# Kernel tuning notes

Hardware: AMD Instinct MI355X
Metric: run time of the kernel (lower is better)

Reference implementation:

```python
import math
import jax, jax.numpy as jnp
import numpy as np

C, H, W, N = 128, 64, 64, 32


def setup_inputs() -> dict:
    key = jax.random.key(0)
    k = jax.random.split(key, 6)
    std = 0.02
    return {
        "x": jax.random.normal(k[0], (N, C, H, W), dtype=jnp.float32),
        # p_3: 1x1 conv, weight [out=C, in=3C]
        "w3": jax.random.normal(k[1], (C, 3 * C), dtype=jnp.float32) * std,
        "p5_w": jax.random.normal(k[2], (1, 1, H, W), dtype=jnp.float32) * std,
        # p_6: conv (3,1), dilation (3,1), weight [O=C, I=C, 3, 1]
        "w6": jax.random.normal(k[3], (C, C, 3, 1), dtype=jnp.float32) * std,
        "p8_w": jax.random.normal(k[4], (1, C, 1, 1), dtype=jnp.float32) * std,
        "p12_w": jax.random.normal(k[5], (1, 1, 3, H, 1), dtype=jnp.float32) * std,
    }


def reference(x, w3, p5_w, w6, p8_w, p12_w):
    n, c, h, w = x.shape
    # F.unfold(x, (1,3), dilation=(1,2), padding=(0,2)) -> taps at w-2, w, w+2 (zero padded)
    xp = jnp.pad(x, ((0, 0), (0, 0), (0, 0), (2, 2)))
    t1 = jnp.stack([xp[..., 0:w], xp[..., 2:w + 2], xp[..., 4:w + 4]], axis=2)  # [n,c,3,h,w]
    t2 = t1.max(axis=2)                                                          # [n,c,h,w]
    # p_3: 1x1 conv over 3c channels
    t3 = jnp.einsum('nkhw,ok->nohw', t1.reshape(n, c * 3, h, w), w3)            # [n,c,h,w]
    t4 = jnp.maximum(t3[:, :, None], t1)                                         # [n,c,3,h,w]
    t5 = p5_w * t2
    # p_6: (3,1) conv, dilation (3,1), padding (3,0) -> same spatial size
    t6 = jax.lax.conv_general_dilated(
        t5, w6, window_strides=(1, 1), padding=((3, 3), (0, 0)),
        rhs_dilation=(3, 1), dimension_numbers=('NCHW', 'OIHW', 'NCHW'))         # [n,c,h,w]
    t7 = jnp.maximum(x, t6)
    t8 = p8_w * t7
    # bmm: [n,c,hw] x [n,hw,3c] -> [n,c,3c]
    t9 = jnp.einsum('ncp,nkp->nck', t8.reshape(n, c, h * w),
                    t1.reshape(n, c * 3, h * w)) / math.sqrt(h * w)
    t10 = t7[:, :, None] + t4                                                    # [n,c,3,h,w]
    t11 = jnp.maximum(t6[:, :, None], t10)                                       # [n,c,3,h,w]
    t12 = p12_w * t11
    # bmm: [n,hw,3c] x [n,3c,c] -> [n,hw,c]
    t13 = jnp.einsum('nkp,nck->npc', t12.reshape(n, c * 3, h * w), t9) / math.sqrt(c * 3)
    return t13.reshape(n, h, w, c).transpose(0, 3, 1, 2)                         # [n,c,h,w]
```

## Files before the change

### kernel.cpp

```cpp
#include <hip/hip_runtime.h>

#define C_   128
#define P_   4096
#define K3   384
#define CP   (C_*P_)
#define NB_  32

typedef __attribute__((ext_vector_type(8))) short short8;
typedef __attribute__((ext_vector_type(4))) short short4v;
typedef __attribute__((ext_vector_type(4))) float f32x4;

__device__ __forceinline__ short f2bf(float f) {
  union { float f; unsigned u; } v; v.f = f;
  unsigned r = v.u + 0x7fffu + ((v.u >> 16) & 1u);
  return (short)(r >> 16);
}
__device__ __forceinline__ float bf2f(short b) {
  union { unsigned u; float f; } v; v.u = ((unsigned)(unsigned short)b) << 16;
  return v.f;
}
__device__ __forceinline__ void gl_lds16(const void* g, void* l) {
  __builtin_amdgcn_global_load_lds(
      (const __attribute__((address_space(1))) unsigned int*)g,
      (__attribute__((address_space(3))) unsigned int*)l, 16, 0, 0);
}

__global__ __launch_bounds__(256) void prep_kernel(const float* __restrict__ w3,
                                                   const float* __restrict__ w6,
                                                   short* __restrict__ w3p,
                                                   short* __restrict__ w6p) {
  int idx = blockIdx.x * 256 + threadIdx.x;
  int m = idx / K3, kp = idx - m * K3;
  int j = kp >> 7, c = kp & 127;
  w3p[idx] = f2bf(w3[m * K3 + c * 3 + j]);
  w6p[idx] = f2bf(w6[m * K3 + c * 3 + j]);
}

__global__ __launch_bounds__(256) void xk_kernel(const float* __restrict__ x,
                                                 short* __restrict__ xb,
                                                 short* __restrict__ xT) {
  int b = blockIdx.x;
  int pt = b & 63, ct = (b >> 6) & 1, n = b >> 7;
  int p0 = pt * 64, c0 = ct * 64;
  const float* xn = x + (size_t)n * CP;
  short* xbn = xb + (size_t)n * CP;
  short* xTn = xT + (size_t)n * CP;
  __shared__ short Ls[64][68];
  int tid = threadIdx.x;
#pragma unroll
  for (int it = 0; it < 4; ++it) {
    int fid = tid + it * 256;
    int i = fid >> 4, j4 = fid & 15;
    f32x4 v = *(const f32x4*)(xn + (c0 + i) * P_ + p0 + j4 * 4);
    short4v s;
#pragma unroll
    for (int r = 0; r < 4; ++r) s[r] = f2bf(v[r]);
    *(short4v*)(xbn + (c0 + i) * P_ + p0 + j4 * 4) = s;
    *(short4v*)(&Ls[i][j4 * 4]) = s;
  }
  __syncthreads();
#pragma unroll
  for (int it = 0; it < 4; ++it) {
    int oid = tid + it * 256;
    int pr = oid >> 4, cg = oid & 15, cb = cg * 4;
    short4v a;
#pragma unroll
    for (int r = 0; r < 4; ++r) a[r] = Ls[cb + r][pr];
    *(short4v*)(xTn + (p0 + pr) * C_ + c0 + cb) = a;
  }
}

__global__ __launch_bounds__(256) void g12_kernel(const short* __restrict__ w3p,
                                                  const short* __restrict__ w6p,
                                                  const float* __restrict__ p5,
                                                  const short* __restrict__ xT,
                                                  short* __restrict__ t3T,
                                                  short* __restrict__ t6T,
                                                  short* __restrict__ t7T) {
  int blk = blockIdx.x;
  int role = blk & 1;
  int b = blk >> 1;
  int n = b >> 5, pt = b & 31, p0 = pt * 128;
  int tid = threadIdx.x, lane = tid & 63, wv = tid >> 6;
  int wm = (wv & 1) * 64, wp = (wv >> 1) * 64;
  const short* Ap = role ? w3p : w6p;
  const short* xTn = xT + (size_t)n * CP;
  __shared__ __align__(16) short As[4][128][8];
  __shared__ __align__(16) short Bs[4][128][8];
  f32x4 acc[4][4] = {};
  for (int ks = 0; ks < 12; ++ks) {
    int k0 = ks * 32;
    int jr = ks >> 2;
    __syncthreads();
#pragma unroll
    for (int it = 0; it < 2; ++it) {
      int slot = tid + it * 256;
      int q = slot >> 7, m = slot & 127;
      gl_lds16(Ap + m * K3 + k0 + q * 8, &As[q][m][0]);
    }
#pragma unroll
    for (int it = 0; it < 2; ++it) {
      int slot = tid + it * 256;
      int q = slot & 3, pc = slot >> 2;
      int p = p0 + pc;
      int c0k = ((ks & 3) * 32) + q * 8;
      short8 zero = {};
      short8 v;
      if (role) {
        int d = 2 * (jr - 1);
        int wd = (p & 63) + d;
        bool valid = (wd >= 0 && wd < 64);
        int prc = min(max(p + d, 0), P_ - 1);
        v = *(const short8*)(xTn + (size_t)prc * C_ + c0k);
        if (!valid) v = zero;
      } else {
        int pr = p + 192 * (jr - 1);
        bool rv = (pr >= 0 && pr < P_);
        int prc = min(max(pr, 0), P_ - 1);
        int w2 = prc & 63;
        const short* rb = xTn + (size_t)prc * C_ + c0k;
        short8 vm = *(const short8*)rb;
        short8 vl = (w2 >= 2) ? *(const short8*)(rb - 2 * C_) : zero;
        short8 vr = (w2 < 62) ? *(const short8*)(rb + 2 * C_) : zero;
        float p5v = p5[prc];
#pragma unroll
        for (int jj = 0; jj < 8; ++jj)
          v[jj] = f2bf(p5v * fmaxf(fmaxf(bf2f(vl[jj]), bf2f(vm[jj])), bf2f(vr[jj])));
        if (!rv) v = zero;
      }
      *(short8*)(&Bs[q][pc][0]) = v;
    }
    __syncthreads();
    int row = lane & 15, q = lane >> 4;
    short8 a[4], bb[4];
#pragma unroll
    for (int im = 0; im < 4; ++im) a[im] = *(const short8*)(&As[q][wm + im * 16 + row][0]);
#pragma unroll
    for (int ip = 0; ip < 4; ++ip) bb[ip] = *(const short8*)(&Bs[q][wp + ip * 16 + row][0]);
#pragma unroll
    for (int im = 0; im < 4; ++im)
#pragma unroll
      for (int ip = 0; ip < 4; ++ip)
        acc[im][ip] = __builtin_amdgcn_mfma_f32_16x16x32_bf16(a[im], bb[ip], acc[im][ip], 0, 0, 0);
  }
  int col = lane & 15, rq = lane >> 4;
  if (role) {
    short* t3Tn = t3T + (size_t)n * CP;
#pragma unroll
    for (int im = 0; im < 4; ++im)
#pragma unroll
      for (int ip = 0; ip < 4; ++ip) {
        int m0 = wm + im * 16 + rq * 4;
        int p = p0 + wp + ip * 16 + col;
        short4v s;
#pragma unroll
        for (int r = 0; r < 4; ++r) s[r] = f2bf(acc[im][ip][r]);
        *(short4v*)(t3Tn + (size_t)p * C_ + m0) = s;
      }
  } else {
    short* t6Tn = t6T + (size_t)n * CP;
    short* t7Tn = t7T + (size_t)n * CP;
#pragma unroll
    for (int im = 0; im < 4; ++im)
#pragma unroll
      for (int ip = 0; ip < 4; ++ip) {
        int m0 = wm + im * 16 + rq * 4;
        int p = p0 + wp + ip * 16 + col;
        short4v ax = *(const short4v*)(xTn + (size_t)p * C_ + m0);
        short4v s6, s7;
#pragma unroll
        for (int r = 0; r < 4; ++r) {
          float t6v = acc[im][ip][r];
          float t7v = fmaxf(bf2f(ax[r]), t6v);
          s6[r] = f2bf(t6v);
          s7[r] = f2bf(t7v);
        }
        *(short4v*)(t6Tn + (size_t)p * C_ + m0) = s6;
        *(short4v*)(t7Tn + (size_t)p * C_ + m0) = s7;
      }
  }
}

__global__ __launch_bounds__(256) void g3_kernel(const short* __restrict__ xb,
                                                 const short* __restrict__ t7T,
                                                 float* __restrict__ t9) {
  int blk = blockIdx.x;
  int nb = blk % 3;
  int tmp = blk / 3;
  int n = tmp & 31, sk = tmp >> 5;
  int d = 2 * (nb - 1);
  int tid = threadIdx.x, lane = tid & 63, wv = tid >> 6;
  int wm = (wv & 1) * 64, wp = (wv >> 1) * 64;
  const short* xbn = xb + (size_t)n * CP;
  const short* t7n = t7T + (size_t)n * CP;
  __shared__ __align__(16) short As[4][128][8];
  __shared__ __align__(16) short Bs[4][128][8];
  f32x4 acc[4][4] = {};
  for (int ks = 0; ks < 16; ++ks) {
    int pp0 = sk * 512 + ks * 32;
    __syncthreads();
#pragma unroll
    for (int it = 0; it < 2; ++it) {
      int slot = tid + it * 256;
      int q = slot >> 7, kc = slot & 127;
      int pb = pp0 + q * 8;
      const int* src = (const int*)(xbn + kc * P_ + pb + d);
      union { int i[4]; short8 s; } u;
#pragma unroll
      for (int t = 0; t < 4; ++t) u.i[t] = src[t];
      short8 v = u.s;
      int w0 = pb & 63;
      if (nb == 0) { if (w0 == 0) { v[0] = 0; v[1] = 0; } }
      else if (nb == 2) { if (w0 == 56) { v[6] = 0; v[7] = 0; } }
      *(short8*)(&As[q][kc][0]) = v;
    }
#pragma unroll
    for (int it = 0; it < 2; ++it) {
      int slot = tid + it * 256;
      int q = slot >> 7, cc = slot & 127;
      const short* bp = t7n + (size_t)(pp0 + q * 8) * C_ + cc;
      short8 v;
#pragma unroll
      for (int j = 0; j < 8; ++j) v[j] = bp[j * C_];
      *(short8*)(&Bs[q][cc][0]) = v;
    }
    __syncthreads();
    int row = lane & 15, q = lane >> 4;
    short8 a[4], bb[4];
#pragma unroll
    for (int im = 0; im < 4; ++im) a[im] = *(const short8*)(&As[q][wm + im * 16 + row][0]);
#pragma unroll
    for (int ip = 0; ip < 4; ++ip) bb[ip] = *(const short8*)(&Bs[q][wp + ip * 16 + row][0]);
#pragma unroll
    for (int im = 0; im < 4; ++im)
#pragma unroll
      for (int ip = 0; ip < 4; ++ip)
        acc[im][ip] = __builtin_amdgcn_mfma_f32_16x16x32_bf16(a[im], bb[ip], acc[im][ip], 0, 0, 0);
  }
  int col = lane & 15, rq = lane >> 4;
  float* t9n = t9 + (size_t)n * (K3 * C_);
#pragma unroll
  for (int im = 0; im < 4; ++im)
#pragma unroll
    for (int ip = 0; ip < 4; ++ip)
#pragma unroll
      for (int r = 0; r < 4; ++r) {
        int kp = nb * 128 + wm + im * 16 + rq * 4 + r;
        int c = wp + ip * 16 + col;
        atomicAdd(&t9n[(size_t)kp * C_ + c], acc[im][ip][r]);
      }
}

__global__ __launch_bounds__(256) void g4_kernel(const float* __restrict__ t9,
                                                 const float* __restrict__ p8,
                                                 const float* __restrict__ p12,
                                                 const short* __restrict__ t3T,
                                                 const short* __restrict__ t6T,
                                                 const short* __restrict__ t7T,
                                                 const short* __restrict__ xT,
                                                 float* __restrict__ out) {
  int b = blockIdx.x;
  int n = b >> 5, pt = b & 31, p0 = pt * 128;
  int tid = threadIdx.x, lane = tid & 63, wv = tid >> 6;
  int wm = (wv & 1) * 64, wp = (wv >> 1) * 64;
  const float* t9n = t9 + (size_t)n * (K3 * C_);
  const short* t3n = t3T + (size_t)n * CP;
  const short* t6n = t6T + (size_t)n * CP;
  const short* t7n = t7T + (size_t)n * CP;
  const short* xTn = xT + (size_t)n * CP;
  const float INV = 1.0f / (64.0f * 19.5959179423f);
  __shared__ __align__(16) short As[4][128][8];
  __shared__ __align__(16) short Bs[4][128][8];
  f32x4 acc[4][4] = {};
  for (int ks = 0; ks < 12; ++ks) {
    int k0 = ks * 32;
    int j = ks >> 2, d = 2 * (j - 1);
    __syncthreads();
#pragma unroll
    for (int it = 0; it < 2; ++it) {
      int slot = tid + it * 256;
      int q = slot >> 7, m = slot & 127;
      float sc = p8[m] * INV;
      short8 v;
#pragma unroll
      for (int jj = 0; jj < 8; ++jj)
        v[jj] = f2bf(t9n[(size_t)(k0 + q * 8 + jj) * C_ + m] * sc);
      *(short8*)(&As[q][m][0]) = v;
    }
#pragma unroll
    for (int it = 0; it < 2; ++it) {
      int slot = tid + it * 256;
      int q = slot & 3, pc = slot >> 2;
      int p = p0 + pc;
      int c0k = ((ks & 3) * 32) + q * 8;
      float s12 = p12[j * 64 + (p >> 6)];
      size_t base = (size_t)p * C_ + c0k;
      short8 a6 = *(const short8*)(t6n + base);
      short8 a7 = *(const short8*)(t7n + base);
      short8 a3 = *(const short8*)(t3n + base);
      int wd = (p & 63) + d;
      bool valid = (wd >= 0 && wd < 64);
      int pr = min(max(p + d, 0), P_ - 1);
      short8 ax = *(const short8*)(xTn + (size_t)pr * C_ + c0k);
      short8 zero = {};
      if (!valid) ax = zero;
      short8 v;
#pragma unroll
      for (int jj = 0; jj < 8; ++jj) {
        float t11 = fmaxf(bf2f(a6[jj]), bf2f(a7[jj]) + fmaxf(bf2f(a3[jj]), bf2f(ax[jj])));
        v[jj] = f2bf(s12 * t11);
      }
      *(short8*)(&Bs[q][pc][0]) = v;
    }
    __syncthreads();
    int row = lane & 15, q = lane >> 4;
    short8 a[4], bb[4];
#pragma unroll
    for (int im = 0; im < 4; ++im) a[im] = *(const short8*)(&As[q][wm + im * 16 + row][0]);
#pragma unroll
    for (int ip = 0; ip < 4; ++ip) bb[ip] = *(const short8*)(&Bs[q][wp + ip * 16 + row][0]);
#pragma unroll
    for (int im = 0; im < 4; ++im)
#pragma unroll
      for (int ip = 0; ip < 4; ++ip)
        acc[im][ip] = __builtin_amdgcn_mfma_f32_16x16x32_bf16(a[im], bb[ip], acc[im][ip], 0, 0, 0);
  }
  int col = lane & 15, rq = lane >> 4;
#pragma unroll
  for (int im = 0; im < 4; ++im)
#pragma unroll
    for (int ip = 0; ip < 4; ++ip)
#pragma unroll
      for (int r = 0; r < 4; ++r) {
        int m = wm + im * 16 + rq * 4 + r;
        int p = p0 + wp + ip * 16 + col;
        out[(size_t)n * CP + m * P_ + p] = acc[im][ip][r];
      }
}

extern "C" void kernel_launch(void* const* d_in, const int* in_sizes, int n_in,
                              void* d_out, int out_size, void* d_ws, size_t ws_size,
                              hipStream_t stream) {
  const float* x   = (const float*)d_in[0];
  const float* w3  = (const float*)d_in[1];
  const float* p5  = (const float*)d_in[2];
  const float* w6  = (const float*)d_in[3];
  const float* p8  = (const float*)d_in[4];
  const float* p12 = (const float*)d_in[5];
  float* out = (float*)d_out;

  char* ws = (char*)d_ws;
  const size_t RB = (size_t)NB_ * CP * 2;
  size_t off = 256;
  short* xb  = (short*)(ws + off); off += RB;
  short* xT  = (short*)(ws + off); off += RB;
  short* t3T = (short*)(ws + off); off += RB;
  short* t6T = (short*)(ws + off); off += RB;
  short* t7T = (short*)(ws + off); off += RB;
  float* t9  = (float*)(ws + off); off += (size_t)NB_ * K3 * C_ * 4;
  short* w3p = (short*)(ws + off); off += 49152 * 2;
  short* w6p = (short*)(ws + off); off += 49152 * 2;

  prep_kernel<<<192, 256, 0, stream>>>(w3, w6, w3p, w6p);
  xk_kernel<<<4096, 256, 0, stream>>>(x, xb, xT);
  g12_kernel<<<2048, 256, 0, stream>>>(w3p, w6p, p5, xT, t3T, t6T, t7T);
  hipMemsetAsync(t9, 0, (size_t)NB_ * K3 * C_ * sizeof(float), stream);
  g3_kernel<<<768, 256, 0, stream>>>(xb, t7T, t9);
  g4_kernel<<<1024, 256, 0, stream>>>(t9, p8, p12, t3T, t6T, t7T, xT, out);
}
```

Baseline: 446.9 us.

## Double-buffer LDS tiles in all GEMM kernels and fold weight prep into xk kernel

Each of the three GEMM kernels now double-buffers its A and B shared-memory tiles. The next k-step's global loads go into registers or are issued as async global-to-LDS copies before the current step's MFMAs, so only one barrier per step is needed. g12's role-1 B path now uses direct global-to-LDS loads, with a zero buffer standing in for padded taps. The separate weight-prep launch is merged into xk_kernel as extra blocks, which removes one launch. In exchange, LDS use doubles to 32KB per block and register pressure rises from the prefetch registers, which may lower occupancy.

```diff
diff --git a/kernel.cpp b/kernel.cpp
--- a/kernel.cpp
+++ b/kernel.cpp
@@ -25,21 +25,40 @@
       (__attribute__((address_space(3))) unsigned int*)l, 16, 0, 0);
 }
 
-__global__ __launch_bounds__(256) void prep_kernel(const float* __restrict__ w3,
-                                                   const float* __restrict__ w6,
-                                                   short* __restrict__ w3p,
-                                                   short* __restrict__ w6p) {
-  int idx = blockIdx.x * 256 + threadIdx.x;
-  int m = idx / K3, kp = idx - m * K3;
-  int j = kp >> 7, c = kp & 127;
-  w3p[idx] = f2bf(w3[m * K3 + c * 3 + j]);
-  w6p[idx] = f2bf(w6[m * K3 + c * 3 + j]);
+__device__ __forceinline__ void mfma_phase(const short (*As_)[128][8],
+                                           const short (*Bs_)[128][8],
+                                           f32x4 acc[4][4], int lane, int wm, int wp) {
+  int row = lane & 15, q = lane >> 4;
+  short8 a[4], bb[4];
+#pragma unroll
+  for (int im = 0; im < 4; ++im) a[im] = *(const short8*)(&As_[q][wm + im * 16 + row][0]);
+#pragma unroll
+  for (int ip = 0; ip < 4; ++ip) bb[ip] = *(const short8*)(&Bs_[q][wp + ip * 16 + row][0]);
+#pragma unroll
+  for (int im = 0; im < 4; ++im)
+#pragma unroll
+    for (int ip = 0; ip < 4; ++ip)
+      acc[im][ip] = __builtin_amdgcn_mfma_f32_16x16x32_bf16(a[im], bb[ip], acc[im][ip], 0, 0, 0);
 }
 
 __global__ __launch_bounds__(256) void xk_kernel(const float* __restrict__ x,
+                                                 const float* __restrict__ w3,
+                                                 const float* __restrict__ w6,
                                                  short* __restrict__ xb,
-                                                 short* __restrict__ xT) {
+                                                 short* __restrict__ xT,
+                                                 short* __restrict__ w3p,
+                                                 short* __restrict__ w6p,
+                                                 short* __restrict__ zbuf) {
   int b = blockIdx.x;
+  if (b >= 4096) {
+    int idx = (b - 4096) * 256 + threadIdx.x;
+    int m = idx / K3, kp = idx - m * K3;
+    int j = kp >> 7, c = kp & 127;
+    w3p[idx] = f2bf(w3[m * K3 + c * 3 + j]);
+    w6p[idx] = f2bf(w6[m * K3 + c * 3 + j]);
+    if (idx < 16) zbuf[idx] = 0;
+    return;
+  }
   int pt = b & 63, ct = (b >> 6) & 1, n = b >> 7;
   int p0 = pt * 64, c0 = ct * 64;
   const float* xn = x + (size_t)n * CP;
@@ -74,6 +93,7 @@
                                                   const short* __restrict__ w6p,
                                                   const float* __restrict__ p5,
                                                   const short* __restrict__ xT,
+                                                  const short* __restrict__ zbuf,
                                                   short* __restrict__ t3T,
                                                   short* __restrict__ t6T,
                                                   short* __restrict__ t7T) {
@@ -85,64 +105,75 @@
   int wm = (wv & 1) * 64, wp = (wv >> 1) * 64;
   const short* Ap = role ? w3p : w6p;
   const short* xTn = xT + (size_t)n * CP;
-  __shared__ __align__(16) short As[4][128][8];
-  __shared__ __align__(16) short Bs[4][128][8];
+  __shared__ __align__(16) short As[2][4][128][8];
+  __shared__ __align__(16) short Bs[2][4][128][8];
   f32x4 acc[4][4] = {};
+  int q_[2], pc_[2];
+#pragma unroll
+  for (int it = 0; it < 2; ++it) { int s = tid + it * 256; q_[it] = s >> 7; pc_[it] = s & 127; }
+
+  short8 rl[2], rm[2], rr[2];
+  float rp5[2];
+
+  auto dmaA = [&](int ks, int buf) {
+#pragma unroll
+    for (int it = 0; it < 2; ++it)
+      gl_lds16(Ap + pc_[it] * K3 + ks * 32 + q_[it] * 8, &As[buf][q_[it]][pc_[it]][0]);
+  };
+  auto dmaB1 = [&](int ks, int buf) {
+    int jr = ks >> 2, d = 2 * (jr - 1);
+#pragma unroll
+    for (int it = 0; it < 2; ++it) {
+      int p = p0 + pc_[it];
+      int c0k = ((ks & 3) * 32) + q_[it] * 8;
+      int wd = (p & 63) + d;
+      bool valid = (wd >= 0 && wd < 64);
+      const short* src = valid ? (xTn + (size_t)(p + d) * C_ + c0k) : zbuf;
+      gl_lds16(src, &Bs[buf][q_[it]][pc_[it]][0]);
+    }
+  };
+  auto preloadB0 = [&](int ks) {
+    int jr = ks >> 2;
+#pragma unroll
+    for (int it = 0; it < 2; ++it) {
+      int p = p0 + pc_[it];
+      int c0k = ((ks & 3) * 32) + q_[it] * 8;
+      int pr = p + 192 * (jr - 1);
+      bool rv = (pr >= 0 && pr < P_);
+      int prc = min(max(pr, 0), P_ - 1);
+      int w2 = prc & 63;
+      const short* rb = xTn + (size_t)prc * C_ + c0k;
+      short8 zero = {};
+      rm[it] = rv ? *(const short8*)rb : zero;
+      rl[it] = (rv && w2 >= 2) ? *(const short8*)(rb - 2 * C_) : zero;
+      rr[it] = (rv && w2 < 62) ? *(const short8*)(rb + 2 * C_) : zero;
+      rp5[it] = rv ? p5[prc] : 0.f;
+    }
+  };
+  auto writeB0 = [&](int buf) {
+#pragma unroll
+    for (int it = 0; it < 2; ++it) {
+      short8 v;
+#pragma unroll
+      for (int jj = 0; jj < 8; ++jj)
+        v[jj] = f2bf(rp5[it] * fmaxf(fmaxf(bf2f(rl[it][jj]), bf2f(rm[it][jj])), bf2f(rr[it][jj])));
+      *(short8*)(&Bs[buf][q_[it]][pc_[it]][0]) = v;
+    }
+  };
+
+  dmaA(0, 0);
+  if (role) dmaB1(0, 0); else preloadB0(0);
+
   for (int ks = 0; ks < 12; ++ks) {
-    int k0 = ks * 32;
-    int jr = ks >> 2;
+    int buf = ks & 1, nbuf = buf ^ 1;
+    if (!role) writeB0(buf);
     __syncthreads();
-#pragma unroll
-    for (int it = 0; it < 2; ++it) {
-      int slot = tid + it * 256;
-      int q = slot >> 7, m = slot & 127;
-      gl_lds16(Ap + m * K3 + k0 + q * 8, &As[q][m][0]);
-    }
-#pragma unroll
-    for (int it = 0; it < 2; ++it) {
-      int slot = tid + it * 256;
-      int q = slot & 3, pc = slot >> 2;
-      int p = p0 + pc;
-      int c0k = ((ks & 3) * 32) + q * 8;
-      short8 zero = {};
-      short8 v;
-      if (role) {
-        int d = 2 * (jr - 1);
-        int wd = (p & 63) + d;
-        bool valid = (wd >= 0 && wd < 64);
-        int prc = min(max(p + d, 0), P_ - 1);
-        v = *(const short8*)(xTn + (size_t)prc * C_ + c0k);
-        if (!valid) v = zero;
-      } else {
-        int pr = p + 192 * (jr - 1);
-        bool rv = (pr >= 0 && pr < P_);
-        int prc = min(max(pr, 0), P_ - 1);
-        int w2 = prc & 63;
-        const short* rb = xTn + (size_t)prc * C_ + c0k;
-        short8 vm = *(const short8*)rb;
-        short8 vl = (w2 >= 2) ? *(const short8*)(rb - 2 * C_) : zero;
-        short8 vr = (w2 < 62) ? *(const short8*)(rb + 2 * C_) : zero;
-        float p5v = p5[prc];
-#pragma unroll
-        for (int jj = 0; jj < 8; ++jj)
-          v[jj] = f2bf(p5v * fmaxf(fmaxf(bf2f(vl[jj]), bf2f(vm[jj])), bf2f(vr[jj])));
-        if (!rv) v = zero;
-      }
-      *(short8*)(&Bs[q][pc][0]) = v;
-    }
-    __syncthreads();
-    int row = lane & 15, q = lane >> 4;
-    short8 a[4], bb[4];
-#pragma unroll
-    for (int im = 0; im < 4; ++im) a[im] = *(const short8*)(&As[q][wm + im * 16 + row][0]);
-#pragma unroll
-    for (int ip = 0; ip < 4; ++ip) bb[ip] = *(const short8*)(&Bs[q][wp + ip * 16 + row][0]);
-#pragma unroll
-    for (int im = 0; im < 4; ++im)
-#pragma unroll
-      for (int ip = 0; ip < 4; ++ip)
-        acc[im][ip] = __builtin_amdgcn_mfma_f32_16x16x32_bf16(a[im], bb[ip], acc[im][ip], 0, 0, 0);
-  }
+    int ksn = (ks + 1 < 12) ? ks + 1 : ks;
+    dmaA(ksn, nbuf);
+    if (role) dmaB1(ksn, nbuf); else preloadB0(ksn);
+    mfma_phase(As[buf], Bs[buf], acc, lane, wm, wp);
+  }
+
   int col = lane & 15, rq = lane >> 4;
   if (role) {
     short* t3Tn = t3T + (size_t)n * CP;
@@ -193,50 +224,74 @@
   int wm = (wv & 1) * 64, wp = (wv >> 1) * 64;
   const short* xbn = xb + (size_t)n * CP;
   const short* t7n = t7T + (size_t)n * CP;
-  __shared__ __align__(16) short As[4][128][8];
-  __shared__ __align__(16) short Bs[4][128][8];
+  __shared__ __align__(16) short As[2][4][128][8];
+  __shared__ __align__(16) short Bs[2][4][128][8];
   f32x4 acc[4][4] = {};
-  for (int ks = 0; ks < 16; ++ks) {
-    int pp0 = sk * 512 + ks * 32;
-    __syncthreads();
-#pragma unroll
-    for (int it = 0; it < 2; ++it) {
-      int slot = tid + it * 256;
-      int q = slot >> 7, kc = slot & 127;
-      int pb = pp0 + q * 8;
-      const int* src = (const int*)(xbn + kc * P_ + pb + d);
+  int q_[2], kc_[2];
+#pragma unroll
+  for (int it = 0; it < 2; ++it) { int s = tid + it * 256; q_[it] = s >> 7; kc_[it] = s & 127; }
+
+  int ra[2][4];
+  short8 rbv[2];
+
+  auto dmaA1 = [&](int ks, int buf) {
+#pragma unroll
+    for (int it = 0; it < 2; ++it)
+      gl_lds16(xbn + kc_[it] * P_ + sk * 512 + ks * 32 + q_[it] * 8,
+               &As[buf][q_[it]][kc_[it]][0]);
+  };
+  auto preloadA = [&](int ks) {
+#pragma unroll
+    for (int it = 0; it < 2; ++it) {
+      int pb = sk * 512 + ks * 32 + q_[it] * 8;
+      const int* src = (const int*)(xbn + kc_[it] * P_ + pb + d);
+#pragma unroll
+      for (int t = 0; t < 4; ++t) ra[it][t] = src[t];
+    }
+  };
+  auto writeA = [&](int ks, int buf) {
+#pragma unroll
+    for (int it = 0; it < 2; ++it) {
       union { int i[4]; short8 s; } u;
 #pragma unroll
-      for (int t = 0; t < 4; ++t) u.i[t] = src[t];
+      for (int t = 0; t < 4; ++t) u.i[t] = ra[it][t];
       short8 v = u.s;
-      int w0 = pb & 63;
+      int w0 = (sk * 512 + ks * 32 + q_[it] * 8) & 63;
       if (nb == 0) { if (w0 == 0) { v[0] = 0; v[1] = 0; } }
       else if (nb == 2) { if (w0 == 56) { v[6] = 0; v[7] = 0; } }
-      *(short8*)(&As[q][kc][0]) = v;
-    }
-#pragma unroll
-    for (int it = 0; it < 2; ++it) {
-      int slot = tid + it * 256;
-      int q = slot >> 7, cc = slot & 127;
-      const short* bp = t7n + (size_t)(pp0 + q * 8) * C_ + cc;
+      *(short8*)(&As[buf][q_[it]][kc_[it]][0]) = v;
+    }
+  };
+  auto preloadB = [&](int ks) {
+#pragma unroll
+    for (int it = 0; it < 2; ++it) {
+      const short* bp = t7n + (size_t)(sk * 512 + ks * 32 + q_[it] * 8) * C_ + kc_[it];
       short8 v;
 #pragma unroll
       for (int j = 0; j < 8; ++j) v[j] = bp[j * C_];
-      *(short8*)(&Bs[q][cc][0]) = v;
-    }
+      rbv[it] = v;
+    }
+  };
+  auto writeB = [&](int buf) {
+#pragma unroll
+    for (int it = 0; it < 2; ++it)
+      *(short8*)(&Bs[buf][q_[it]][kc_[it]][0]) = rbv[it];
+  };
+
+  if (nb == 1) dmaA1(0, 0); else preloadA(0);
+  preloadB(0);
+
+  for (int ks = 0; ks < 16; ++ks) {
+    int buf = ks & 1, nbuf = buf ^ 1;
+    if (nb != 1) writeA(ks, buf);
+    writeB(buf);
     __syncthreads();
-    int row = lane & 15, q = lane >> 4;
-    short8 a[4], bb[4];
-#pragma unroll
-    for (int im = 0; im < 4; ++im) a[im] = *(const short8*)(&As[q][wm + im * 16 + row][0]);
-#pragma unroll
-    for (int ip = 0; ip < 4; ++ip) bb[ip] = *(const short8*)(&Bs[q][wp + ip * 16 + row][0]);
-#pragma unroll
-    for (int im = 0; im < 4; ++im)
-#pragma unroll
-      for (int ip = 0; ip < 4; ++ip)
-        acc[im][ip] = __builtin_amdgcn_mfma_f32_16x16x32_bf16(a[im], bb[ip], acc[im][ip], 0, 0, 0);
-  }
+    int ksn = (ks + 1 < 16) ? ks + 1 : ks;
+    if (nb == 1) dmaA1(ksn, nbuf); else preloadA(ksn);
+    preloadB(ksn);
+    mfma_phase(As[buf], Bs[buf], acc, lane, wm, wp);
+  }
+
   int col = lane & 15, rq = lane >> 4;
   float* t9n = t9 + (size_t)n * (K3 * C_);
 #pragma unroll
@@ -269,62 +324,83 @@
   const short* t7n = t7T + (size_t)n * CP;
   const short* xTn = xT + (size_t)n * CP;
   const float INV = 1.0f / (64.0f * 19.5959179423f);
-  __shared__ __align__(16) short As[4][128][8];
-  __shared__ __align__(16) short Bs[4][128][8];
+  __shared__ __align__(16) short As[2][4][128][8];
+  __shared__ __align__(16) short Bs[2][4][128][8];
   f32x4 acc[4][4] = {};
-  for (int ks = 0; ks < 12; ++ks) {
-    int k0 = ks * 32;
+  int q_[2], m_[2];
+#pragma unroll
+  for (int it = 0; it < 2; ++it) { int s = tid + it * 256; q_[it] = s >> 7; m_[it] = s & 127; }
+  float psc[2];
+#pragma unroll
+  for (int it = 0; it < 2; ++it) psc[it] = p8[m_[it]] * INV;
+
+  float raf[2][8];
+  short8 rb6[2], rb7[2], rb3[2], rbx[2];
+  float rs12[2];
+
+  auto preloadA = [&](int ks) {
+#pragma unroll
+    for (int it = 0; it < 2; ++it)
+#pragma unroll
+      for (int jj = 0; jj < 8; ++jj)
+        raf[it][jj] = t9n[(size_t)(ks * 32 + q_[it] * 8 + jj) * C_ + m_[it]];
+  };
+  auto writeA = [&](int buf) {
+#pragma unroll
+    for (int it = 0; it < 2; ++it) {
+      short8 v;
+#pragma unroll
+      for (int jj = 0; jj < 8; ++jj) v[jj] = f2bf(raf[it][jj] * psc[it]);
+      *(short8*)(&As[buf][q_[it]][m_[it]][0]) = v;
+    }
+  };
+  auto preloadB = [&](int ks) {
     int j = ks >> 2, d = 2 * (j - 1);
-    __syncthreads();
-#pragma unroll
-    for (int it = 0; it < 2; ++it) {
-      int slot = tid + it * 256;
-      int q = slot >> 7, m = slot & 127;
-      float sc = p8[m] * INV;
-      short8 v;
-#pragma unroll
-      for (int jj = 0; jj < 8; ++jj)
-        v[jj] = f2bf(t9n[(size_t)(k0 + q * 8 + jj) * C_ + m] * sc);
-      *(short8*)(&As[q][m][0]) = v;
-    }
-#pragma unroll
-    for (int it = 0; it < 2; ++it) {
-      int slot = tid + it * 256;
-      int q = slot & 3, pc = slot >> 2;
-      int p = p0 + pc;
-      int c0k = ((ks & 3) * 32) + q * 8;
-      float s12 = p12[j * 64 + (p >> 6)];
+#pragma unroll
+    for (int it = 0; it < 2; ++it) {
+      int p = p0 + m_[it];
+      int c0k = ((ks & 3) * 32) + q_[it] * 8;
       size_t base = (size_t)p * C_ + c0k;
-      short8 a6 = *(const short8*)(t6n + base);
-      short8 a7 = *(const short8*)(t7n + base);
-      short8 a3 = *(const short8*)(t3n + base);
+      rb6[it] = *(const short8*)(t6n + base);
+      rb7[it] = *(const short8*)(t7n + base);
+      rb3[it] = *(const short8*)(t3n + base);
       int wd = (p & 63) + d;
       bool valid = (wd >= 0 && wd < 64);
       int pr = min(max(p + d, 0), P_ - 1);
       short8 ax = *(const short8*)(xTn + (size_t)pr * C_ + c0k);
       short8 zero = {};
-      if (!valid) ax = zero;
+      rbx[it] = valid ? ax : zero;
+      rs12[it] = p12[j * 64 + (p >> 6)];
+    }
+  };
+  auto writeB = [&](int buf) {
+#pragma unroll
+    for (int it = 0; it < 2; ++it) {
       short8 v;
 #pragma unroll
       for (int jj = 0; jj < 8; ++jj) {
-        float t11 = fmaxf(bf2f(a6[jj]), bf2f(a7[jj]) + fmaxf(bf2f(a3[jj]), bf2f(ax[jj])));
-        v[jj] = f2bf(s12 * t11);
+        float t11 = fmaxf(bf2f(rb6[it][jj]),
+                          bf2f(rb7[it][jj]) + fmaxf(bf2f(rb3[it][jj]), bf2f(rbx[it][jj])));
+        v[jj] = f2bf(rs12[it] * t11);
       }
-      *(short8*)(&Bs[q][pc][0]) = v;
-    }
+      *(short8*)(&Bs[buf][q_[it]][m_[it]][0]) = v;
+    }
+  };
+
+  preloadA(0);
+  preloadB(0);
+
+  for (int ks = 0; ks < 12; ++ks) {
+    int buf = ks & 1, nbuf = buf ^ 1;
+    writeA(buf);
+    writeB(buf);
     __syncthreads();
-    int row = lane & 15, q = lane >> 4;
-    short8 a[4], bb[4];
-#pragma unroll
-    for (int im = 0; im < 4; ++im) a[im] = *(const short8*)(&As[q][wm + im * 16 + row][0]);
-#pragma unroll
-    for (int ip = 0; ip < 4; ++ip) bb[ip] = *(const short8*)(&Bs[q][wp + ip * 16 + row][0]);
-#pragma unroll
-    for (int im = 0; im < 4; ++im)
-#pragma unroll
-      for (int ip = 0; ip < 4; ++ip)
-        acc[im][ip] = __builtin_amdgcn_mfma_f32_16x16x32_bf16(a[im], bb[ip], acc[im][ip], 0, 0, 0);
-  }
+    int ksn = (ks + 1 < 12) ? ks + 1 : ks;
+    preloadA(ksn);
+    preloadB(ksn);
+    mfma_phase(As[buf], Bs[buf], acc, lane, wm, wp);
+  }
+
   int col = lane & 15, rq = lane >> 4;
 #pragma unroll
   for (int im = 0; im < 4; ++im)
@@ -360,11 +436,11 @@
   float* t9  = (float*)(ws + off); off += (size_t)NB_ * K3 * C_ * 4;
   short* w3p = (short*)(ws + off); off += 49152 * 2;
   short* w6p = (short*)(ws + off); off += 49152 * 2;
-
-  prep_kernel<<<192, 256, 0, stream>>>(w3, w6, w3p, w6p);
-  xk_kernel<<<4096, 256, 0, stream>>>(x, xb, xT);
-  g12_kernel<<<2048, 256, 0, stream>>>(w3p, w6p, p5, xT, t3T, t6T, t7T);
+  short* zbuf = (short*)(ws + off); off += 64;
+
+  xk_kernel<<<4288, 256, 0, stream>>>(x, w3, w6, xb, xT, w3p, w6p, zbuf);
   hipMemsetAsync(t9, 0, (size_t)NB_ * K3 * C_ * sizeof(float), stream);
+  g12_kernel<<<2048, 256, 0, stream>>>(w3p, w6p, p5, xT, zbuf, t3T, t6T, t7T);
   g3_kernel<<<768, 256, 0, stream>>>(xb, t7T, t9);
   g4_kernel<<<1024, 256, 0, stream>>>(t9, p8, p12, t3T, t6T, t7T, xT, out);
 }
```

New measurement: 473.7 us. +6.0%, slower.
